# Kernel optimization log

Measured on AMD Instinct MI355X. Metric: run time of the kernel, lower is better.

## Reference

```python
import jax, jax.numpy as jnp
import numpy as np

B, E, T, N = 1024, 512, 8, 256


def setup_inputs() -> dict:
    key = jax.random.key(0)
    k1, k2, k3, k4 = jax.random.split(key, 4)
    weights = jax.random.uniform(k1, (T,), dtype=jnp.float32)  # one scalar per bond type
    bond_src = jax.random.randint(k2, (B, E), 0, N - 1, dtype=jnp.int32)  # raw i, offset +1 later
    bond_dst = jax.random.randint(k3, (B, E), 0, N - 1, dtype=jnp.int32)
    bond_type = jax.random.randint(k4, (B, E), 0, T, dtype=jnp.int32)
    return {"weights": weights, "bond_src": bond_src, "bond_dst": bond_dst,
            "bond_type": bond_type, "num_nodes": N}


def reference(weights, bond_src, bond_dst, bond_type, num_nodes):
    # Gather per-bond weight, then symmetric scatter into dense [B, N, N] adjacency.
    batch, n_edges = bond_src.shape
    w = weights[bond_type]                                  # [B, E] gather
    bidx = jnp.broadcast_to(jnp.arange(batch)[:, None], (batch, n_edges))
    src = bond_src + 1                                      # +1 node offset as in torch code
    dst = bond_dst + 1
    bond_matrix = jnp.zeros((batch, num_nodes, num_nodes), dtype=weights.dtype)
    bond_matrix = bond_matrix.at[bidx, src, dst].set(w)
    bond_matrix = bond_matrix.at[bidx, dst, src].set(w)
    return bond_matrix
```

## Files before the change

### kernel.cpp

```cpp
#include <hip/hip_runtime.h>


#define NB_E 512
#define NB_N 256

__global__ __launch_bounds__(256) void BondWeight_41738492182540_kernel(
    const float* __restrict__ weights,
    const int*   __restrict__ bsrc,
    const int*   __restrict__ bdst,
    const int*   __restrict__ btyp,
    float*       __restrict__ out)
{
    __shared__ int   s_off1[NB_E];
    __shared__ int   s_off2[NB_E];
    __shared__ float s_w[NB_E];

    const int b = blockIdx.x;
    const int t = threadIdx.x;
    float* __restrict__ tile = out + (size_t)b * (NB_N * NB_N);

    const int ebase = b * NB_E;
    #pragma unroll
    for (int i = 0; i < NB_E / 256; ++i) {
        const int e  = t + 256 * i;
        const int si = bsrc[ebase + e] + 1;
        const int di = bdst[ebase + e] + 1;
        const int ty = btyp[ebase + e] & 7;
        const float w = weights[ty];
        s_off1[e] = si * NB_N + di;
        s_off2[e] = di * NB_N + si;
        s_w[e]    = w;
    }

    const float4 z = make_float4(0.f, 0.f, 0.f, 0.f);
    float4* __restrict__ tile4 = (float4*)tile;
    #pragma unroll 8
    for (int k = 0; k < 64; ++k)
        tile4[t + 256 * k] = z;

    __syncthreads();

    if (t == 0) {
        #pragma unroll 8
        for (int e = 0; e < NB_E; ++e)
            tile[s_off1[e]] = s_w[e];
        #pragma unroll 8
        for (int e = 0; e < NB_E; ++e)
            tile[s_off2[e]] = s_w[e];
    }
}

extern "C" void kernel_launch(void* const* d_in, const int* in_sizes, int n_in,
                              void* d_out, int out_size, void* d_ws, size_t ws_size,
                              hipStream_t stream) {
    const float* weights = (const float*)d_in[0];
    const int*   bsrc    = (const int*)d_in[1];
    const int*   bdst    = (const int*)d_in[2];
    const int*   btyp    = (const int*)d_in[3];
    float*       out     = (float*)d_out;

    const int nb = in_sizes[1] / NB_E;

    BondWeight_41738492182540_kernel<<<nb, 256, 0, stream>>>(
        weights, bsrc, bdst, btyp, out);
}
```

Baseline: 312.6 us.

## Build adjacency tiles in LDS with parallel max-sequence scatter, then stream out

Replaces the single-thread serial scatter into global memory with a parallel scheme. Each block builds 64-row chunks of its adjacency matrix in LDS as packed 16-bit cells holding a sequence number and bond type. A CAS-based max keeps the last-write-wins order of the reference. Each chunk is then decoded to weights and written with full-width nontemporal stores, so the separate global zeroing pass and the serialized scattered writes disappear. In exchange it adds LDS atomics, four chunk passes with barriers, and a per-cell weight lookup.

```diff
diff --git a/kernel.cpp b/kernel.cpp
--- a/kernel.cpp
+++ b/kernel.cpp
@@ -3,6 +3,25 @@
 
 #define NB_E 512
 #define NB_N 256
+#define CH_ROWS 64
+#define CH_WORDS (CH_ROWS * NB_N / 2)
+
+typedef float v4f __attribute__((ext_vector_type(4)));
+
+__device__ __forceinline__ void lds_max_u16(unsigned int* tab, int cell, unsigned int v16)
+{
+    unsigned int* w = tab + (cell >> 1);
+    const int sh = (cell & 1) * 16;
+    unsigned int old = *w;
+    while (true) {
+        const unsigned int cur = (old >> sh) & 0xFFFFu;
+        if (cur >= v16) break;
+        const unsigned int nw = (old & ~(0xFFFFu << sh)) | (v16 << sh);
+        const unsigned int seen = atomicCAS(w, old, nw);
+        if (seen == old) break;
+        old = seen;
+    }
+}
 
 __global__ __launch_bounds__(256) void BondWeight_41738492182540_kernel(
     const float* __restrict__ weights,
@@ -11,42 +30,58 @@
     const int*   __restrict__ btyp,
     float*       __restrict__ out)
 {
-    __shared__ int   s_off1[NB_E];
-    __shared__ int   s_off2[NB_E];
-    __shared__ float s_w[NB_E];
+    __shared__ unsigned int seqtab[CH_WORDS];
+    __shared__ float s_wt[8];
 
     const int b = blockIdx.x;
     const int t = threadIdx.x;
-    float* __restrict__ tile = out + (size_t)b * (NB_N * NB_N);
+
+    if (t < 8) s_wt[t] = weights[t];
 
     const int ebase = b * NB_E;
+    int row[4], col[4];
+    unsigned int pk[4];
     #pragma unroll
-    for (int i = 0; i < NB_E / 256; ++i) {
+    for (int i = 0; i < 2; ++i) {
         const int e  = t + 256 * i;
-        const int si = bsrc[ebase + e] + 1;
-        const int di = bdst[ebase + e] + 1;
-        const int ty = btyp[ebase + e] & 7;
-        const float w = weights[ty];
-        s_off1[e] = si * NB_N + di;
-        s_off2[e] = di * NB_N + si;
-        s_w[e]    = w;
+        const int s1 = bsrc[ebase + e] + 1;
+        const int d1 = bdst[ebase + e] + 1;
+        const unsigned int ty = (unsigned int)btyp[ebase + e] & 7u;
+        row[2*i]   = s1; col[2*i]   = d1; pk[2*i]   = ((unsigned int)(e + 1) << 3) | ty;
+        row[2*i+1] = d1; col[2*i+1] = s1; pk[2*i+1] = ((unsigned int)(NB_E + e + 1) << 3) | ty;
     }
 
-    const float4 z = make_float4(0.f, 0.f, 0.f, 0.f);
-    float4* __restrict__ tile4 = (float4*)tile;
-    #pragma unroll 8
-    for (int k = 0; k < 64; ++k)
-        tile4[t + 256 * k] = z;
+    float4* __restrict__ out4 = ((float4*)out) + (size_t)b * (NB_N * NB_N / 4);
 
-    __syncthreads();
+    for (int r0 = 0; r0 < NB_N; r0 += CH_ROWS) {
+        uint4* tab4 = (uint4*)seqtab;
+        #pragma unroll
+        for (int k = 0; k < CH_WORDS / 4 / 256; ++k)
+            tab4[t + 256 * k] = make_uint4(0u, 0u, 0u, 0u);
+        __syncthreads();
 
-    if (t == 0) {
-        #pragma unroll 8
-        for (int e = 0; e < NB_E; ++e)
-            tile[s_off1[e]] = s_w[e];
-        #pragma unroll 8
-        for (int e = 0; e < NB_E; ++e)
-            tile[s_off2[e]] = s_w[e];
+        #pragma unroll
+        for (int i = 0; i < 4; ++i) {
+            const int r = row[i] - r0;
+            if (0 <= r && r < CH_ROWS)
+                lds_max_u16(seqtab, r * NB_N + col[i], pk[i]);
+        }
+        __syncthreads();
+
+        #pragma unroll
+        for (int k = 0; k < (CH_ROWS * NB_N / 4) / 256; ++k) {
+            const int i4 = t + 256 * k;
+            const unsigned int a  = seqtab[2 * i4];
+            const unsigned int bb = seqtab[2 * i4 + 1];
+            v4f v;
+            unsigned int p;
+            p = a & 0xFFFFu;  v.x = p ? s_wt[p & 7u] : 0.0f;
+            p = a >> 16;      v.y = p ? s_wt[p & 7u] : 0.0f;
+            p = bb & 0xFFFFu; v.z = p ? s_wt[p & 7u] : 0.0f;
+            p = bb >> 16;     v.w = p ? s_wt[p & 7u] : 0.0f;
+            __builtin_nontemporal_store(v, (v4f*)&out4[r0 * (NB_N / 4) + i4]);
+        }
+        __syncthreads();
     }
 }
 
```

Result: faster. 278.6 us (-10.9%).
